# Kernel optimization log

Hardware: AMD Instinct MI355X
Metric: run time of the kernel (lower is better)

## Reference

```python
import jax, jax.numpy as jnp
import numpy as np

EPS_F = 1e-12
M, N = 64, 4096  # feature dim m, num nodes n


def setup_inputs() -> dict:
    key = jax.random.key(0)
    k1, k2, k3, k4 = jax.random.split(key, 4)
    # X: (m, n) node features transposed, as in the repo (features.t())
    X = jax.random.normal(k1, (M, N), dtype=jnp.float32)
    # F: (m, m) parameter, xavier_uniform init
    bound = float(np.sqrt(6.0 / (M + M)))
    F = jax.random.uniform(k2, (M, M), minval=-bound, maxval=bound, dtype=jnp.float32)
    # Q_S: (n, n) orthogonal eigenvector matrix of the (symmetric, normalized) adjacency
    A = jax.random.normal(k3, (N, N), dtype=jnp.float32)
    Q_S, _ = jnp.linalg.qr(A)
    Q_S = Q_S.astype(jnp.float32)
    # Lambda_S: (n, 1) eigenvalues of normalized adjacency, inside (-1, 1)
    Lambda_S = jnp.sort(
        jax.random.uniform(k4, (N, 1), minval=-0.95, maxval=0.95, dtype=jnp.float32), axis=0
    )
    gamma = jnp.asarray(0.8, dtype=jnp.float32)
    return {"X": X, "F": F, "Q_S": Q_S, "Lambda_S": Lambda_S, "gamma": gamma}


def reference(X, F, Q_S, Lambda_S, gamma):
    # g(F) = F^T F / (||F^T F||_F + eps)  -- Frobenius-normalized Gram matrix
    FF = F.T @ F                                   # (m, m)
    G_F = FF / (jnp.linalg.norm(FF) + EPS_F)       # (m, m), symmetric PSD, ||.||_F ~ 1
    # spectral decomposition of g(F)
    Lambda_F, Q_F = jnp.linalg.eigh(G_F)           # (m,), (m, m)
    # closed-form equilibrium of Z = gamma * g(F) Z S^T + X in the joint eigenbasis
    D = 1.0 / (1.0 - gamma * Lambda_F[:, None] * Lambda_S.reshape(1, -1))  # (m, n)
    Z = Q_F @ (D * (Q_F.T @ X @ Q_S)) @ Q_S.T      # (m, n)
    return Z
```

## Files before the change

### kernel.cpp

```cpp
#include <hip/hip_runtime.h>
#include <math.h>


typedef short short8 __attribute__((ext_vector_type(8)));
typedef float floatx16 __attribute__((ext_vector_type(16)));

#define KSPLIT 16
#define KCHUNK 256
constexpr int Mdim = 64;
constexpr int Ndim = 4096;

__device__ inline ushort f2bf(float f) {
    uint u = __float_as_uint(f);
    u += 0x7fff + ((u >> 16) & 1);
    return (ushort)(u >> 16);
}
__device__ inline float bf2f(ushort h) { return __uint_as_float(((uint)h) << 16); }

__device__ inline floatx16 mfma_bf16(short8 a, short8 b, floatx16 c) {
    return __builtin_amdgcn_mfma_f32_32x32x16_bf16(a, b, c, 0, 0, 0);
}

struct SharedGemm { ushort Ah[4096], Al[4096], Bh[4096]; };
struct SharedPrep { float Fraw[64 * 65]; ushort Ph[4096], Pl[4096]; float red[256]; };
union SharedU { SharedGemm g; SharedPrep p; };

__global__ __launch_bounds__(256) void init_kernel(float* __restrict__ W, float* __restrict__ Z) {
    const int i = blockIdx.x * 256 + threadIdx.x;
    float4 z = {0.f, 0.f, 0.f, 0.f};
    if (i < 65536) *(float4*)&W[i * 4] = z;
    else *(float4*)&Z[(i - 65536) * 4] = z;
}

__device__ void prep_body(SharedPrep& sp, const float* __restrict__ F, float* __restrict__ Gout) {
    const int t = threadIdx.x;
    const int l = t & 63, w = t >> 6;
    const int tm = w & 1, tn = w >> 1;
    const int am = tm * 32 + (l & 31);
    const int bn = tn * 32 + (l & 31);
    const int lk = l >> 5;

    for (int s = 0; s < 4; ++s) {
        int e = t + 256 * s;
        int r = e >> 4, q = (e & 15) * 4;
        float4 v = *(const float4*)&F[r * 64 + q];
        float fa[4] = {v.x, v.y, v.z, v.w};
        for (int i = 0; i < 4; ++i) sp.Fraw[r * 65 + q + i] = fa[i];
    }
    __syncthreads();
    {
        int c = t >> 2, kbase = (t & 3) * 16;
        ushort hh[16], ll[16];
#pragma unroll
        for (int kk = 0; kk < 16; ++kk) {
            float v = sp.Fraw[(kbase + kk) * 65 + c];
            ushort h = f2bf(v);
            hh[kk] = h;
            ll[kk] = f2bf(v - bf2f(h));
        }
#pragma unroll
        for (int g = 0; g < 2; ++g) {
            int gk = (kbase >> 3) + g;
            int idx = c * 64 + ((gk ^ (c & 7)) * 8);
#pragma unroll
            for (int u = 0; u < 8; ++u) { sp.Ph[idx + u] = hh[8 * g + u]; sp.Pl[idx + u] = ll[8 * g + u]; }
        }
    }
    __syncthreads();
    floatx16 acc;
    for (int i = 0; i < 16; ++i) acc[i] = 0.f;
    for (int s16 = 0; s16 < 4; ++s16) {
        int gk = 2 * s16 + lk;
        int ai = am * 64 + ((gk ^ (am & 7)) * 8);
        int bi = bn * 64 + ((gk ^ (bn & 7)) * 8);
        short8 ah = *(const short8*)&sp.Ph[ai];
        short8 al = *(const short8*)&sp.Pl[ai];
        short8 bh = *(const short8*)&sp.Ph[bi];
        short8 bl = *(const short8*)&sp.Pl[bi];
        acc = mfma_bf16(ah, bh, acc);
        acc = mfma_bf16(al, bh, acc);
        acc = mfma_bf16(ah, bl, acc);
    }
    float ss = 0.f;
    for (int r = 0; r < 16; ++r) ss += acc[r] * acc[r];
    sp.red[t] = ss;
    __syncthreads();
    for (int off = 128; off > 0; off >>= 1) {
        if (t < off) sp.red[t] += sp.red[t + off];
        __syncthreads();
    }
    const float inv = 1.0f / (sqrtf(sp.red[0]) + 1e-12f);
    for (int r = 0; r < 16; ++r) {
        int row = (r & 3) + 8 * (r >> 2) + 4 * lk + tm * 32;
        int col = tn * 32 + (l & 31);
        float v = acc[r] * inv;
        Gout[row * 64 + col] = v;
        ushort h = f2bf(v);
        int idx = row * 64 + (((col >> 3) ^ (row & 7)) * 8 + (col & 7));
        sp.Ph[idx] = h;
        sp.Pl[idx] = f2bf(v - bf2f(h));
    }
    for (int j = 1; j < 5; ++j) {
        __syncthreads();
        floatx16 a2;
        for (int i = 0; i < 16; ++i) a2[i] = 0.f;
        for (int s16 = 0; s16 < 4; ++s16) {
            int gk = 2 * s16 + lk;
            int ai = am * 64 + ((gk ^ (am & 7)) * 8);
            int bi = bn * 64 + ((gk ^ (bn & 7)) * 8);
            short8 ah = *(const short8*)&sp.Ph[ai];
            short8 al = *(const short8*)&sp.Pl[ai];
            short8 bh = *(const short8*)&sp.Ph[bi];
            short8 bl = *(const short8*)&sp.Pl[bi];
            a2 = mfma_bf16(ah, bh, a2);
            a2 = mfma_bf16(al, bh, a2);
            a2 = mfma_bf16(ah, bl, a2);
        }
        __syncthreads();
        for (int r = 0; r < 16; ++r) {
            int row = (r & 3) + 8 * (r >> 2) + 4 * lk + tm * 32;
            int col = tn * 32 + (l & 31);
            float v = a2[r];
            Gout[j * 4096 + row * 64 + col] = v;
            ushort h = f2bf(v);
            int idx = row * 64 + (((col >> 3) ^ (row & 7)) * 8 + (col & 7));
            sp.Ph[idx] = h;
            sp.Pl[idx] = f2bf(v - bf2f(h));
        }
    }
}

template <bool TB, bool DOPREP>
__global__ __launch_bounds__(256, 4) void gemm_kernel(const float* __restrict__ A,
                                                      const float* __restrict__ Bm,
                                                      float* __restrict__ C,
                                                      const float* __restrict__ F,
                                                      float* __restrict__ Gp) {
    __shared__ SharedU sh;
    const int bid = blockIdx.x;
    if (DOPREP) {
        if (bid == 0) { prep_body(sh.p, F, Gp); return; }
    }
    const int b = DOPREP ? bid - 1 : bid;
    const int n0 = (b & 63) * 64;
    const int kb = (b >> 6) * KCHUNK;
    const int t = threadIdx.x;
    const int l = t & 63, w = t >> 6;
    const int tm = w & 1, tn = w >> 1;
    const int am = tm * 32 + (l & 31);
    const int bn = tn * 32 + (l & 31);
    const int lk = l >> 5;
    const int sr = t >> 2, sj = t & 3;
    const int nq = t & 15, kr2 = 2 * (t >> 4);

    floatx16 acc;
    for (int i = 0; i < 16; ++i) acc[i] = 0.f;

    float4 bbuf[2][4];
#pragma unroll
    for (int p = 0; p < 2; ++p) {
        const int kp = kb + p * 64;
        if (TB) {
#pragma unroll
            for (int s = 0; s < 4; ++s)
                bbuf[p][s] = *(const float4*)&Bm[(size_t)(n0 + sr) * 4096 + kp + 4 * sj + 16 * s];
        } else {
#pragma unroll
            for (int s = 0; s < 2; ++s) {
                bbuf[p][2 * s + 0] = *(const float4*)&Bm[(size_t)(kp + kr2 + 32 * s) * 4096 + n0 + 4 * nq];
                bbuf[p][2 * s + 1] = *(const float4*)&Bm[(size_t)(kp + kr2 + 1 + 32 * s) * 4096 + n0 + 4 * nq];
            }
        }
    }

#pragma unroll
    for (int step = 0; step < KCHUNK / 64; ++step) {
        const int k0 = kb + step * 64;
        const int cur = step & 1;
        float4 av[4];
#pragma unroll
        for (int s = 0; s < 4; ++s)
            av[s] = *(const float4*)&A[sr * 4096 + k0 + 4 * sj + 16 * s];
        __syncthreads();
        if (TB) {
#pragma unroll
            for (int s = 0; s < 4; ++s) {
                int off = 4 * sj + 16 * s;
                int idx = sr * 64 + (((off >> 3) ^ (sr & 7)) * 8 + (off & 7));
                float fb[4] = {bbuf[cur][s].x, bbuf[cur][s].y, bbuf[cur][s].z, bbuf[cur][s].w};
                ushort4 h4;
                ushort* hp = (ushort*)&h4;
#pragma unroll
                for (int i = 0; i < 4; ++i) hp[i] = f2bf(fb[i]);
                *(ushort4*)&sh.g.Bh[idx] = h4;
            }
        } else {
#pragma unroll
            for (int s = 0; s < 2; ++s) {
                int k = kr2 + 32 * s;
                float fa[4] = {bbuf[cur][2 * s].x, bbuf[cur][2 * s].y, bbuf[cur][2 * s].z, bbuf[cur][2 * s].w};
                float fb[4] = {bbuf[cur][2 * s + 1].x, bbuf[cur][2 * s + 1].y, bbuf[cur][2 * s + 1].z, bbuf[cur][2 * s + 1].w};
#pragma unroll
                for (int i = 0; i < 4; ++i) {
                    int n = 4 * nq + i;
                    int idx = n * 64 + (((k >> 3) ^ (n & 7)) * 8 + (k & 7));
                    ushort2 hp2;
                    hp2.x = f2bf(fa[i]);
                    hp2.y = f2bf(fb[i]);
                    *(ushort2*)&sh.g.Bh[idx] = hp2;
                }
            }
        }
        if (step + 2 < KCHUNK / 64) {
            const int k2 = k0 + 128;
            if (TB) {
#pragma unroll
                for (int s = 0; s < 4; ++s)
                    bbuf[cur][s] = *(const float4*)&Bm[(size_t)(n0 + sr) * 4096 + k2 + 4 * sj + 16 * s];
            } else {
#pragma unroll
                for (int s = 0; s < 2; ++s) {
                    bbuf[cur][2 * s + 0] = *(const float4*)&Bm[(size_t)(k2 + kr2 + 32 * s) * 4096 + n0 + 4 * nq];
                    bbuf[cur][2 * s + 1] = *(const float4*)&Bm[(size_t)(k2 + kr2 + 1 + 32 * s) * 4096 + n0 + 4 * nq];
                }
            }
        }
#pragma unroll
        for (int s = 0; s < 4; ++s) {
            int off = 4 * sj + 16 * s;
            int idx = sr * 64 + (((off >> 3) ^ (sr & 7)) * 8 + (off & 7));
            float fa[4] = {av[s].x, av[s].y, av[s].z, av[s].w};
            ushort4 h4, l4;
            ushort* hp = (ushort*)&h4; ushort* lp = (ushort*)&l4;
#pragma unroll
            for (int i = 0; i < 4; ++i) {
                uint u = __float_as_uint(fa[i]);
                float lo = fa[i] - __uint_as_float(u & 0xffff0000u);
                hp[i] = (ushort)(u >> 16);
                lp[i] = (ushort)(__float_as_uint(lo) >> 16);
            }
            *(ushort4*)&sh.g.Ah[idx] = h4;
            *(ushort4*)&sh.g.Al[idx] = l4;
        }
        __syncthreads();
#pragma unroll
        for (int s16 = 0; s16 < 4; ++s16) {
            int gk = 2 * s16 + lk;
            int ai = am * 64 + ((gk ^ (am & 7)) * 8);
            int bi = bn * 64 + ((gk ^ (bn & 7)) * 8);
            short8 ah = *(const short8*)&sh.g.Ah[ai];
            short8 al = *(const short8*)&sh.g.Al[ai];
            short8 bh = *(const short8*)&sh.g.Bh[bi];
            acc = mfma_bf16(ah, bh, acc);
            acc = mfma_bf16(al, bh, acc);
        }
    }
    const int colg = n0 + tn * 32 + (l & 31);
#pragma unroll
    for (int r = 0; r < 16; ++r) {
        int row = (r & 3) + 8 * (r >> 2) + 4 * lk + tm * 32;
        atomicAdd(&C[row * 4096 + colg], acc[r]);
    }
}

__global__ __launch_bounds__(256) void solve_kernel(const float* __restrict__ W,
                                                    const float* __restrict__ Gp,
                                                    const float* __restrict__ lam,
                                                    const float* __restrict__ gammap,
                                                    float* __restrict__ Y) {
    __shared__ float Gs[64][68];
    __shared__ float T[64][17];
    const int t = threadIdx.x;
    const int c0 = blockIdx.x * 16;
    for (int e = t; e < 1024; e += 256)
        T[e >> 4][e & 15] = W[(e >> 4) * 4096 + c0 + (e & 15)];
    const int tx = t & 15;
    const int r4 = (t >> 4) * 4;
    const float a = gammap[0] * lam[c0 + tx];
    float s = a;
    for (int j = 0; j < 5; ++j) {
        __syncthreads();
        for (int e = t; e < 4096; e += 256) Gs[e >> 6][e & 63] = Gp[j * 4096 + e];
        __syncthreads();
        float u0 = 0.f, u1 = 0.f, u2 = 0.f, u3 = 0.f;
#pragma unroll 8
        for (int k = 0; k < 64; ++k) {
            const float tv = T[k][tx];
            const float4 g = *(const float4*)&Gs[k][r4];
            u0 += g.x * tv; u1 += g.y * tv; u2 += g.z * tv; u3 += g.w * tv;
        }
        __syncthreads();
        T[r4 + 0][tx] += s * u0;
        T[r4 + 1][tx] += s * u1;
        T[r4 + 2][tx] += s * u2;
        T[r4 + 3][tx] += s * u3;
        s = s * s;
    }
    __syncthreads();
    for (int e = t; e < 1024; e += 256)
        Y[(e >> 4) * 4096 + c0 + (e & 15)] = T[e >> 4][e & 15];
}

extern "C" void kernel_launch(void* const* d_in, const int* in_sizes, int n_in,
                              void* d_out, int out_size, void* d_ws, size_t ws_size,
                              hipStream_t stream) {
    const float* X     = (const float*)d_in[0];
    const float* F     = (const float*)d_in[1];
    const float* Qs    = (const float*)d_in[2];
    const float* lam   = (const float*)d_in[3];
    const float* gamma = (const float*)d_in[4];
    float* Z = (float*)d_out;

    float* W  = (float*)d_ws;
    float* Y  = W + Mdim * Ndim;
    float* Gp = Y + Mdim * Ndim;

    init_kernel<<<512, 256, 0, stream>>>(W, Z);
    gemm_kernel<false, true><<<64 * KSPLIT + 1, 256, 0, stream>>>(X, Qs, W, F, Gp);
    solve_kernel<<<Ndim / 16, 256, 0, stream>>>(W, Gp, lam, gamma, Y);
    gemm_kernel<true, false><<<64 * KSPLIT, 256, 0, stream>>>(Y, Qs, Z, nullptr, nullptr);
}
```

Baseline: 161.0 us.

## Pre-split operands to bf16 in global memory and stage via direct global-to-LDS loads

```diff
diff --git a/kernel.cpp b/kernel.cpp
--- a/kernel.cpp
+++ b/kernel.cpp
@@ -21,15 +21,40 @@
     return __builtin_amdgcn_mfma_f32_32x32x16_bf16(a, b, c, 0, 0, 0);
 }
 
+__device__ inline void gl_lds16(const ushort* g, ushort* l) {
+    __builtin_amdgcn_global_load_lds(
+        (const __attribute__((address_space(1))) void*)g,
+        (__attribute__((address_space(3))) void*)l,
+        16, 0, 0);
+}
+
 struct SharedGemm { ushort Ah[4096], Al[4096], Bh[4096]; };
 struct SharedPrep { float Fraw[64 * 65]; ushort Ph[4096], Pl[4096]; float red[256]; };
 union SharedU { SharedGemm g; SharedPrep p; };
 
-__global__ __launch_bounds__(256) void init_kernel(float* __restrict__ W, float* __restrict__ Z) {
+__global__ __launch_bounds__(256) void init_kernel(const float* __restrict__ X,
+                                                   float* __restrict__ W, float* __restrict__ Z,
+                                                   ushort* __restrict__ Xh, ushort* __restrict__ Xl) {
     const int i = blockIdx.x * 256 + threadIdx.x;
     float4 z = {0.f, 0.f, 0.f, 0.f};
-    if (i < 65536) *(float4*)&W[i * 4] = z;
-    else *(float4*)&Z[(i - 65536) * 4] = z;
+    if (i < 65536) {
+        *(float4*)&W[i * 4] = z;
+        float4 v = *(const float4*)&X[i * 4];
+        float fa[4] = {v.x, v.y, v.z, v.w};
+        ushort4 h4, l4;
+        ushort* hp = (ushort*)&h4; ushort* lp = (ushort*)&l4;
+#pragma unroll
+        for (int j = 0; j < 4; ++j) {
+            uint u = __float_as_uint(fa[j]);
+            float lo = fa[j] - __uint_as_float(u & 0xffff0000u);
+            hp[j] = (ushort)(u >> 16);
+            lp[j] = (ushort)(__float_as_uint(lo) >> 16);
+        }
+        *(ushort4*)&Xh[i * 4] = h4;
+        *(ushort4*)&Xl[i * 4] = l4;
+    } else {
+        *(float4*)&Z[(i - 65536) * 4] = z;
+    }
 }
 
 __device__ void prep_body(SharedPrep& sp, const float* __restrict__ F, float* __restrict__ Gout) {
@@ -130,18 +155,17 @@
     }
 }
 
-template <bool TB, bool DOPREP>
-__global__ __launch_bounds__(256, 4) void gemm_kernel(const float* __restrict__ A,
-                                                      const float* __restrict__ Bm,
-                                                      float* __restrict__ C,
-                                                      const float* __restrict__ F,
-                                                      float* __restrict__ Gp) {
+__global__ __launch_bounds__(256, 4) void gemm1_kernel(const ushort* __restrict__ Xh,
+                                                       const ushort* __restrict__ Xl,
+                                                       const float* __restrict__ Qs,
+                                                       float* __restrict__ W,
+                                                       const float* __restrict__ F,
+                                                       float* __restrict__ Gp,
+                                                       ushort* __restrict__ Qbf) {
     __shared__ SharedU sh;
     const int bid = blockIdx.x;
-    if (DOPREP) {
-        if (bid == 0) { prep_body(sh.p, F, Gp); return; }
-    }
-    const int b = DOPREP ? bid - 1 : bid;
+    if (bid == 0) { prep_body(sh.p, F, Gp); return; }
+    const int b = bid - 1;
     const int n0 = (b & 63) * 64;
     const int kb = (b >> 6) * KCHUNK;
     const int t = threadIdx.x;
@@ -150,8 +174,8 @@
     const int am = tm * 32 + (l & 31);
     const int bn = tn * 32 + (l & 31);
     const int lk = l >> 5;
-    const int sr = t >> 2, sj = t & 3;
     const int nq = t & 15, kr2 = 2 * (t >> 4);
+    const int dn = t >> 3, dg = t & 7;
 
     floatx16 acc;
     for (int i = 0; i < 16; ++i) acc[i] = 0.f;
@@ -160,16 +184,10 @@
 #pragma unroll
     for (int p = 0; p < 2; ++p) {
         const int kp = kb + p * 64;
-        if (TB) {
-#pragma unroll
-            for (int s = 0; s < 4; ++s)
-                bbuf[p][s] = *(const float4*)&Bm[(size_t)(n0 + sr) * 4096 + kp + 4 * sj + 16 * s];
-        } else {
-#pragma unroll
-            for (int s = 0; s < 2; ++s) {
-                bbuf[p][2 * s + 0] = *(const float4*)&Bm[(size_t)(kp + kr2 + 32 * s) * 4096 + n0 + 4 * nq];
-                bbuf[p][2 * s + 1] = *(const float4*)&Bm[(size_t)(kp + kr2 + 1 + 32 * s) * 4096 + n0 + 4 * nq];
-            }
+#pragma unroll
+        for (int s = 0; s < 2; ++s) {
+            bbuf[p][2 * s + 0] = *(const float4*)&Qs[(size_t)(kp + kr2 + 32 * s) * 4096 + n0 + 4 * nq];
+            bbuf[p][2 * s + 1] = *(const float4*)&Qs[(size_t)(kp + kr2 + 1 + 32 * s) * 4096 + n0 + 4 * nq];
         }
     }
 
@@ -177,77 +195,48 @@
     for (int step = 0; step < KCHUNK / 64; ++step) {
         const int k0 = kb + step * 64;
         const int cur = step & 1;
-        float4 av[4];
-#pragma unroll
-        for (int s = 0; s < 4; ++s)
-            av[s] = *(const float4*)&A[sr * 4096 + k0 + 4 * sj + 16 * s];
-        __syncthreads();
-        if (TB) {
-#pragma unroll
-            for (int s = 0; s < 4; ++s) {
-                int off = 4 * sj + 16 * s;
-                int idx = sr * 64 + (((off >> 3) ^ (sr & 7)) * 8 + (off & 7));
-                float fb[4] = {bbuf[cur][s].x, bbuf[cur][s].y, bbuf[cur][s].z, bbuf[cur][s].w};
-                ushort4 h4;
-                ushort* hp = (ushort*)&h4;
-#pragma unroll
-                for (int i = 0; i < 4; ++i) hp[i] = f2bf(fb[i]);
-                *(ushort4*)&sh.g.Bh[idx] = h4;
+        __syncthreads();
+#pragma unroll
+        for (int r = 0; r < 2; ++r) {
+            const int m = dn + 32 * r;
+            const int g = dg ^ (m & 7);
+            gl_lds16(&Xh[(size_t)m * 4096 + k0 + g * 8], &sh.g.Ah[w * 512 + r * 2048]);
+            gl_lds16(&Xl[(size_t)m * 4096 + k0 + g * 8], &sh.g.Al[w * 512 + r * 2048]);
+        }
+#pragma unroll
+        for (int s = 0; s < 2; ++s) {
+            const int k = kr2 + 32 * s;
+            float fa[4] = {bbuf[cur][2 * s].x, bbuf[cur][2 * s].y, bbuf[cur][2 * s].z, bbuf[cur][2 * s].w};
+            float fb[4] = {bbuf[cur][2 * s + 1].x, bbuf[cur][2 * s + 1].y, bbuf[cur][2 * s + 1].z, bbuf[cur][2 * s + 1].w};
+            ushort4 qa, qb;
+            ushort* qap = (ushort*)&qa; ushort* qbp = (ushort*)&qb;
+#pragma unroll
+            for (int i = 0; i < 4; ++i) {
+                const int n = 4 * nq + i;
+                const int idx = n * 64 + (((k >> 3) ^ (n & 7)) * 8 + (k & 7));
+                ushort2 hp2;
+                hp2.x = f2bf(fa[i]);
+                hp2.y = f2bf(fb[i]);
+                *(ushort2*)&sh.g.Bh[idx] = hp2;
+                qap[i] = hp2.x; qbp[i] = hp2.y;
             }
-        } else {
-#pragma unroll
-            for (int s = 0; s < 2; ++s) {
-                int k = kr2 + 32 * s;
-                float fa[4] = {bbuf[cur][2 * s].x, bbuf[cur][2 * s].y, bbuf[cur][2 * s].z, bbuf[cur][2 * s].w};
-                float fb[4] = {bbuf[cur][2 * s + 1].x, bbuf[cur][2 * s + 1].y, bbuf[cur][2 * s + 1].z, bbuf[cur][2 * s + 1].w};
-#pragma unroll
-                for (int i = 0; i < 4; ++i) {
-                    int n = 4 * nq + i;
-                    int idx = n * 64 + (((k >> 3) ^ (n & 7)) * 8 + (k & 7));
-                    ushort2 hp2;
-                    hp2.x = f2bf(fa[i]);
-                    hp2.y = f2bf(fb[i]);
-                    *(ushort2*)&sh.g.Bh[idx] = hp2;
-                }
-            }
+            *(ushort4*)&Qbf[(size_t)(k0 + k) * 4096 + n0 + 4 * nq] = qa;
+            *(ushort4*)&Qbf[(size_t)(k0 + k + 1) * 4096 + n0 + 4 * nq] = qb;
         }
         if (step + 2 < KCHUNK / 64) {
             const int k2 = k0 + 128;
-            if (TB) {
-#pragma unroll
-                for (int s = 0; s < 4; ++s)
-                    bbuf[cur][s] = *(const float4*)&Bm[(size_t)(n0 + sr) * 4096 + k2 + 4 * sj + 16 * s];
-            } else {
-#pragma unroll
-                for (int s = 0; s < 2; ++s) {
-                    bbuf[cur][2 * s + 0] = *(const float4*)&Bm[(size_t)(k2 + kr2 + 32 * s) * 4096 + n0 + 4 * nq];
-                    bbuf[cur][2 * s + 1] = *(const float4*)&Bm[(size_t)(k2 + kr2 + 1 + 32 * s) * 4096 + n0 + 4 * nq];
-                }
+#pragma unroll
+            for (int s = 0; s < 2; ++s) {
+                bbuf[cur][2 * s + 0] = *(const float4*)&Qs[(size_t)(k2 + kr2 + 32 * s) * 4096 + n0 + 4 * nq];
+                bbuf[cur][2 * s + 1] = *(const float4*)&Qs[(size_t)(k2 + kr2 + 1 + 32 * s) * 4096 + n0 + 4 * nq];
             }
         }
-#pragma unroll
-        for (int s = 0; s < 4; ++s) {
-            int off = 4 * sj + 16 * s;
-            int idx = sr * 64 + (((off >> 3) ^ (sr & 7)) * 8 + (off & 7));
-            float fa[4] = {av[s].x, av[s].y, av[s].z, av[s].w};
-            ushort4 h4, l4;
-            ushort* hp = (ushort*)&h4; ushort* lp = (ushort*)&l4;
-#pragma unroll
-            for (int i = 0; i < 4; ++i) {
-                uint u = __float_as_uint(fa[i]);
-                float lo = fa[i] - __uint_as_float(u & 0xffff0000u);
-                hp[i] = (ushort)(u >> 16);
-                lp[i] = (ushort)(__float_as_uint(lo) >> 16);
-            }
-            *(ushort4*)&sh.g.Ah[idx] = h4;
-            *(ushort4*)&sh.g.Al[idx] = l4;
-        }
         __syncthreads();
 #pragma unroll
         for (int s16 = 0; s16 < 4; ++s16) {
-            int gk = 2 * s16 + lk;
-            int ai = am * 64 + ((gk ^ (am & 7)) * 8);
-            int bi = bn * 64 + ((gk ^ (bn & 7)) * 8);
+            const int gk = 2 * s16 + lk;
+            const int ai = am * 64 + ((gk ^ (am & 7)) * 8);
+            const int bi = bn * 64 + ((gk ^ (bn & 7)) * 8);
             short8 ah = *(const short8*)&sh.g.Ah[ai];
             short8 al = *(const short8*)&sh.g.Al[ai];
             short8 bh = *(const short8*)&sh.g.Bh[bi];
@@ -259,7 +248,7 @@
 #pragma unroll
     for (int r = 0; r < 16; ++r) {
         int row = (r & 3) + 8 * (r >> 2) + 4 * lk + tm * 32;
-        atomicAdd(&C[row * 4096 + colg], acc[r]);
+        atomicAdd(&W[row * 4096 + colg], acc[r]);
     }
 }
 
@@ -267,7 +256,8 @@
                                                     const float* __restrict__ Gp,
                                                     const float* __restrict__ lam,
                                                     const float* __restrict__ gammap,
-                                                    float* __restrict__ Y) {
+                                                    ushort* __restrict__ Yh,
+                                                    ushort* __restrict__ Yl) {
     __shared__ float Gs[64][68];
     __shared__ float T[64][17];
     const int t = threadIdx.x;
@@ -297,8 +287,66 @@
         s = s * s;
     }
     __syncthreads();
-    for (int e = t; e < 1024; e += 256)
-        Y[(e >> 4) * 4096 + c0 + (e & 15)] = T[e >> 4][e & 15];
+    for (int e = t; e < 1024; e += 256) {
+        const int r = e >> 4, cc = e & 15;
+        const float v = T[r][cc];
+        const uint u = __float_as_uint(v);
+        const float lo = v - __uint_as_float(u & 0xffff0000u);
+        Yh[r * 4096 + c0 + cc] = (ushort)(u >> 16);
+        Yl[r * 4096 + c0 + cc] = (ushort)(__float_as_uint(lo) >> 16);
+    }
+}
+
+__global__ __launch_bounds__(256, 4) void gemm2_kernel(const ushort* __restrict__ Yh,
+                                                       const ushort* __restrict__ Yl,
+                                                       const ushort* __restrict__ Qbf,
+                                                       float* __restrict__ Z) {
+    __shared__ SharedU sh;
+    const int b = blockIdx.x;
+    const int n0 = (b & 63) * 64;
+    const int kb = (b >> 6) * KCHUNK;
+    const int t = threadIdx.x;
+    const int l = t & 63, w = t >> 6;
+    const int tm = w & 1, tn = w >> 1;
+    const int am = tm * 32 + (l & 31);
+    const int bn = tn * 32 + (l & 31);
+    const int lk = l >> 5;
+    const int dn = t >> 3, dg = t & 7;
+
+    floatx16 acc;
+    for (int i = 0; i < 16; ++i) acc[i] = 0.f;
+
+#pragma unroll
+    for (int step = 0; step < KCHUNK / 64; ++step) {
+        const int k0 = kb + step * 64;
+        __syncthreads();
+#pragma unroll
+        for (int r = 0; r < 2; ++r) {
+            const int m = dn + 32 * r;
+            const int g = dg ^ (m & 7);
+            gl_lds16(&Yh[(size_t)m * 4096 + k0 + g * 8], &sh.g.Ah[w * 512 + r * 2048]);
+            gl_lds16(&Yl[(size_t)m * 4096 + k0 + g * 8], &sh.g.Al[w * 512 + r * 2048]);
+            gl_lds16(&Qbf[(size_t)(n0 + m) * 4096 + k0 + g * 8], &sh.g.Bh[w * 512 + r * 2048]);
+        }
+        __syncthreads();
+#pragma unroll
+        for (int s16 = 0; s16 < 4; ++s16) {
+            const int gk = 2 * s16 + lk;
+            const int ai = am * 64 + ((gk ^ (am & 7)) * 8);
+            const int bi = bn * 64 + ((gk ^ (bn & 7)) * 8);
+            short8 ah = *(const short8*)&sh.g.Ah[ai];
+            short8 al = *(const short8*)&sh.g.Al[ai];
+            short8 bh = *(const short8*)&sh.g.Bh[bi];
+            acc = mfma_bf16(ah, bh, acc);
+            acc = mfma_bf16(al, bh, acc);
+        }
+    }
+    const int colg = n0 + tn * 32 + (l & 31);
+#pragma unroll
+    for (int r = 0; r < 16; ++r) {
+        int row = (r & 3) + 8 * (r >> 2) + 4 * lk + tm * 32;
+        atomicAdd(&Z[row * 4096 + colg], acc[r]);
+    }
 }
 
 extern "C" void kernel_launch(void* const* d_in, const int* in_sizes, int n_in,
@@ -311,12 +359,16 @@
     const float* gamma = (const float*)d_in[4];
     float* Z = (float*)d_out;
 
-    float* W  = (float*)d_ws;
-    float* Y  = W + Mdim * Ndim;
-    float* Gp = Y + Mdim * Ndim;
-
-    init_kernel<<<512, 256, 0, stream>>>(W, Z);
-    gemm_kernel<false, true><<<64 * KSPLIT + 1, 256, 0, stream>>>(X, Qs, W, F, Gp);
-    solve_kernel<<<Ndim / 16, 256, 0, stream>>>(W, Gp, lam, gamma, Y);
-    gemm_kernel<true, false><<<64 * KSPLIT, 256, 0, stream>>>(Y, Qs, Z, nullptr, nullptr);
-}
+    float*  W   = (float*)d_ws;
+    float*  Gp  = W + 262144;
+    ushort* Xh  = (ushort*)(Gp + 20480);
+    ushort* Xl  = Xh + 262144;
+    ushort* Yh  = Xl + 262144;
+    ushort* Yl  = Yh + 262144;
+    ushort* Qbf = Yl + 262144;
+
+    init_kernel<<<512, 256, 0, stream>>>(X, W, Z, Xh, Xl);
+    gemm1_kernel<<<64 * KSPLIT + 1, 256, 0, stream>>>(Xh, Xl, Qs, W, F, Gp, Qbf);
+    solve_kernel<<<Ndim / 16, 256, 0, stream>>>(W, Gp, lam, gamma, Yh, Yl);
+    gemm2_kernel<<<64 * KSPLIT, 256, 0, stream>>>(Yh, Yl, Qbf, Z);
+}
```

Result: no change. 160.6 us (-0.2%).
